# Kernel tuning notes

Hardware: AMD Instinct MI355X
Metric: run time of the kernel (lower is better)

The kernel has to match this reference:

```python
import jax, jax.numpy as jnp
import numpy as np
from jax import lax

N, D, NUM_SPEC, NUM_HOPS = 8192, 256, 32, 3
ETA, EPS, LN_EPS = 0.5, 0.5, 1e-5


def setup_inputs() -> dict:
    key = jax.random.key(0)
    ks = jax.random.split(key, 4)
    H = jax.random.normal(ks[0], (N, D), dtype=jnp.float32)
    # normalized adjacency proxy: scale so spectral norm is O(1) and hops stay stable
    A = jax.random.normal(ks[1], (N, N), dtype=jnp.float32) / jnp.sqrt(jnp.float32(N))
    # orthonormal-ish eigenvector columns
    V = jax.random.normal(ks[2], (N, NUM_SPEC), dtype=jnp.float32)
    V = V / jnp.linalg.norm(V, axis=0, keepdims=True)
    eigvals = jax.random.uniform(ks[3], (NUM_SPEC,), dtype=jnp.float32, maxval=2.0)
    return {
        "H": H,
        "A": A,
        "V": V,
        "eigvals": eigvals,
        "spec_logits": jnp.zeros((NUM_SPEC,), jnp.float32),
        "lap_logits": jnp.full((NUM_SPEC,), 0.1, jnp.float32),
        "hop_weights": jnp.full((NUM_HOPS + 1,), 1.0 / (NUM_HOPS + 1), jnp.float32),
        "threshold": jnp.full((D,), 0.05, jnp.float32),
        "ln_gamma": jnp.ones((D,), jnp.float32),
        "ln_beta": jnp.zeros((D,), jnp.float32),
    }


def reference(H, A, V, eigvals, spec_logits, lap_logits, hop_weights, threshold, ln_gamma, ln_beta):
    n, d = H.shape
    num_hops = hop_weights.shape[0] - 1

    # hop propagation: hops[k] = A^k H, shape [K, n, d] with K = num_hops+1
    def step(Hc, _):
        Hn = A @ Hc
        return Hn, Hn
    _, rest = lax.scan(step, H, None, length=num_hops)
    hops = jnp.concatenate([H[None], rest], axis=0)  # [K, n, d]

    hop_w = jax.nn.softmax(hop_weights)          # [K]
    spec_w = jax.nn.softmax(spec_logits)         # [S]
    lap_lams = jax.nn.softplus(lap_logits)       # [S]
    coeff = jnp.float32(d) / (jnp.float32(n) * jnp.float32(EPS) ** 2)

    # Phi[k,s,:] = v_s^T H_k  -> batched rank-1 projections
    Phi = jnp.einsum('ns,knd->ksd', V, hops)     # [K, S, d]

    # M = I + coeff * phi phi^T, batched small [d,d] SPD solves
    eye = jnp.eye(d, dtype=H.dtype)
    M = eye + coeff * jnp.einsum('ksi,ksj->ksij', Phi, Phi)  # [K,S,d,d]
    # phi @ M^{-1} == M^{-1} phi (M symmetric)
    q = coeff * jnp.linalg.solve(M, Phi[..., None])[..., 0]  # [K,S,d]

    # grad_R_total = sum_{k,s} hop_w[k] spec_w[s] v_s q_{k,s}^T = V @ T_R
    T_R = spec_w[:, None] * jnp.einsum('k,ksd->sd', hop_w, q)       # [S,d]
    grad_R = V @ T_R                                                 # [n,d]

    # grad_L_total = sum_{k,s} hop_w[k] lap_lams[s] eig_s v_s phi_{k,s}^T
    T_L = (lap_lams * eigvals)[:, None] * jnp.einsum('k,ksd->sd', hop_w, Phi)
    grad_L = V @ T_L

    H_half = H + ETA * grad_R - ETA * grad_L

    # soft threshold (proximal L1)
    thr = threshold[None, :]
    H_out = jnp.sign(H_half) * jax.nn.relu(jnp.abs(H_half) - thr)

    # LayerNorm over last dim
    mu = jnp.mean(H_out, axis=-1, keepdims=True)
    var = jnp.var(H_out, axis=-1, keepdims=True)
    H_out = (H_out - mu) / jnp.sqrt(var + LN_EPS) * ln_gamma + ln_beta
    return (H_out, lax.stop_gradient(hop_w), lax.stop_gradient(spec_w))
```

## Files before the change

### kernel.cpp

```cpp
#include <hip/hip_runtime.h>
#include <hip/hip_bf16.h>
#include <stdint.h>

#define NN 8192
#define DIM 256
#define NSPEC 32
#define ETA 0.5f
#define COEFF 0.125f
#define LNEPS 1e-5f

typedef __attribute__((ext_vector_type(8))) short bf16x8;
typedef __attribute__((ext_vector_type(4))) float f32x4;

__device__ __forceinline__ unsigned short bf2u(__hip_bfloat16 b) {
    union { __hip_bfloat16 b; unsigned short u; } c; c.b = b; return c.u;
}
__device__ __forceinline__ __hip_bfloat16 u2bf(unsigned short u) {
    union { __hip_bfloat16 b; unsigned short u; } c; c.u = u; return c.b;
}
__device__ __forceinline__ float bfbits2f(unsigned short u) {
    union { unsigned int i; float f; } c; c.i = ((unsigned int)u) << 16; return c.f;
}

__device__ __forceinline__ void async16(const void* g, void* l) {
    __builtin_amdgcn_global_load_lds(
        (const __attribute__((address_space(1))) void*)g,
        (__attribute__((address_space(3))) void*)l, 16, 0, 0);
}

__global__ void cast_A(const float4* __restrict__ src, ushort4* __restrict__ dst, int n4) {
    int i = blockIdx.x * 256 + threadIdx.x;
    int stride = gridDim.x * 256;
    for (int j = i; j < n4; j += stride) {
        float4 v = src[j];
        ushort4 o;
        o.x = bf2u(__float2bfloat16(v.x));
        o.y = bf2u(__float2bfloat16(v.y));
        o.z = bf2u(__float2bfloat16(v.z));
        o.w = bf2u(__float2bfloat16(v.w));
        dst[j] = o;
    }
}

__global__ void cast_trans(const float* __restrict__ X, __hip_bfloat16* __restrict__ Xbf,
                           __hip_bfloat16* __restrict__ XT) {
    __shared__ unsigned short tile[64 * 66];
    int r0 = blockIdx.x * 64, c0 = blockIdx.y * 64;
    int t = threadIdx.x;
    for (int i = 0; i < 16; ++i) {
        int idx = i * 256 + t;
        int r = idx >> 6, c = idx & 63;
        float v = X[(long)(r0 + r) * DIM + c0 + c];
        __hip_bfloat16 b = __float2bfloat16(v);
        Xbf[(long)(r0 + r) * DIM + c0 + c] = b;
        tile[r * 66 + c] = bf2u(b);
    }
    __syncthreads();
    for (int i = 0; i < 16; ++i) {
        int idx = i * 256 + t;
        int c = idx >> 6, r = idx & 63;
        XT[(long)(c0 + c) * NN + r0 + r] = u2bf(tile[r * 66 + c]);
    }
}

#define BM 128
#define BN 128
#define BK 64
#define KSPLIT 4
#define KC (NN / KSPLIT)
#define KITERS (KC / BK)

__launch_bounds__(256, 2)
__global__ void gemm_splitk(const __hip_bfloat16* __restrict__ A,
                            const __hip_bfloat16* __restrict__ BT,
                            float* __restrict__ P) {
    __shared__ __align__(16) __hip_bfloat16 As[2][BM * BK];
    __shared__ __align__(16) __hip_bfloat16 Bs[2][BN * BK];
    const int t = threadIdx.x;
    const int w = t >> 6, l = t & 63;
    const int wm = w & 1, wn = w >> 1;
    const long gm0 = (long)blockIdx.x * BM;
    const long gn0 = (long)blockIdx.y * BN;
    const long kbase = (long)blockIdx.z * KC;

    const int lr = l >> 3;
    const int lg = l & 7;
    const int glog = lg ^ lr;

    auto stage = [&](int buf, long kpos) {
#pragma unroll
        for (int c = 0; c < 4; ++c) {
            int rb = w * 32 + c * 8;
            async16(A + (gm0 + rb + lr) * (long)NN + kpos + glog * 8, &As[buf][rb * BK]);
        }
#pragma unroll
        for (int c = 0; c < 4; ++c) {
            int rb = w * 32 + c * 8;
            async16(BT + (gn0 + rb + lr) * (long)NN + kpos + glog * 8, &Bs[buf][rb * BK]);
        }
    };

    f32x4 acc[4][4];
#pragma unroll
    for (int mt = 0; mt < 4; ++mt)
#pragma unroll
        for (int nt = 0; nt < 4; ++nt)
            acc[mt][nt] = (f32x4){0.f, 0.f, 0.f, 0.f};

    const int rowq = l & 15;
    const int kq = l >> 4;

    stage(0, kbase);
    for (int kt = 0; kt < KITERS; ++kt) {
        __syncthreads();
        const int cur = kt & 1;
        if (kt + 1 < KITERS) stage(cur ^ 1, kbase + (long)(kt + 1) * BK);

#pragma unroll
        for (int ks = 0; ks < 2; ++ks) {
            const int kg = kq + ks * 4;
            bf16x8 af[4], bfr[4];
#pragma unroll
            for (int mt = 0; mt < 4; ++mt) {
                int m = wm * 64 + mt * 16 + rowq;
                af[mt] = *(const bf16x8*)&As[cur][m * BK + ((kg ^ (m & 7)) << 3)];
            }
#pragma unroll
            for (int nt = 0; nt < 4; ++nt) {
                int n = wn * 64 + nt * 16 + rowq;
                bfr[nt] = *(const bf16x8*)&Bs[cur][n * BK + ((kg ^ (n & 7)) << 3)];
            }
#pragma unroll
            for (int mt = 0; mt < 4; ++mt)
#pragma unroll
                for (int nt = 0; nt < 4; ++nt)
                    acc[mt][nt] = __builtin_amdgcn_mfma_f32_16x16x32_bf16(
                        af[mt], bfr[nt], acc[mt][nt], 0, 0, 0);
        }
    }

    float* Pz = P + (long)blockIdx.z * NN * DIM;
#pragma unroll
    for (int mt = 0; mt < 4; ++mt)
#pragma unroll
        for (int nt = 0; nt < 4; ++nt)
#pragma unroll
            for (int r = 0; r < 4; ++r) {
                long m = gm0 + wm * 64 + mt * 16 + (l >> 4) * 4 + r;
                long n = gn0 + wn * 64 + nt * 16 + (l & 15);
                Pz[m * DIM + n] = acc[mt][nt][r];
            }
}

__global__ void reduce_ct(const float* __restrict__ P, __hip_bfloat16* __restrict__ Xbf,
                          __hip_bfloat16* __restrict__ XT, int writeT) {
    __shared__ unsigned short tile[64 * 66];
    int r0 = blockIdx.x * 64, c0 = blockIdx.y * 64;
    int t = threadIdx.x;
    const long S = (long)NN * DIM;
    for (int i = 0; i < 16; ++i) {
        int idx = i * 256 + t;
        int r = idx >> 6, c = idx & 63;
        long off = (long)(r0 + r) * DIM + c0 + c;
        float v = P[off] + P[S + off] + P[2 * S + off] + P[3 * S + off];
        __hip_bfloat16 b = __float2bfloat16(v);
        Xbf[off] = b;
        tile[r * 66 + c] = bf2u(b);
    }
    __syncthreads();
    if (writeT) {
        for (int i = 0; i < 16; ++i) {
            int idx = i * 256 + t;
            int c = idx >> 6, r = idx & 63;
            XT[(long)(c0 + c) * NN + r0 + r] = u2bf(tile[r * 66 + c]);
        }
    }
}

__global__ void phi_kernel(const float* __restrict__ V,
                           const __hip_bfloat16* __restrict__ X0,
                           const __hip_bfloat16* __restrict__ X1,
                           const __hip_bfloat16* __restrict__ X2,
                           const __hip_bfloat16* __restrict__ X3,
                           float* __restrict__ Phi) {
    __shared__ float ldsV[64 * NSPEC];
    int t = threadIdx.x;
    int s0 = (t >> 6) * 8;
    int d0 = (t & 63) * 4;
    int n0 = blockIdx.x * 128;
    int k = blockIdx.y;
    const __hip_bfloat16* X = (k == 0) ? X0 : (k == 1) ? X1 : (k == 2) ? X2 : X3;
    float4 acc[8];
#pragma unroll
    for (int j = 0; j < 8; ++j) acc[j] = (float4){0.f, 0.f, 0.f, 0.f};

    for (int tile = 0; tile < 2; ++tile) {
        int nb = n0 + tile * 64;
#pragma unroll
        for (int i = 0; i < 8; ++i) {
            int idx = i * 256 + t;
            int r = idx >> 5, c = idx & 31;
            ldsV[idx] = V[(long)(nb + r) * NSPEC + c];
        }
        __syncthreads();
        for (int nn = 0; nn < 64; ++nn) {
            ushort4 xu = *(const ushort4*)&X[(long)(nb + nn) * DIM + d0];
            float x0 = bfbits2f(xu.x), x1 = bfbits2f(xu.y), x2 = bfbits2f(xu.z), x3 = bfbits2f(xu.w);
#pragma unroll
            for (int j = 0; j < 8; ++j) {
                float vs = ldsV[nn * NSPEC + s0 + j];
                acc[j].x += vs * x0; acc[j].y += vs * x1;
                acc[j].z += vs * x2; acc[j].w += vs * x3;
            }
        }
        __syncthreads();
    }
#pragma unroll
    for (int j = 0; j < 8; ++j) {
        float* ph = &Phi[((k * NSPEC) + s0 + j) * DIM + d0];
        atomicAdd(ph + 0, acc[j].x);
        atomicAdd(ph + 1, acc[j].y);
        atomicAdd(ph + 2, acc[j].z);
        atomicAdd(ph + 3, acc[j].w);
    }
}

__global__ void tc_kernel(const float* __restrict__ Phi,
                          const float* __restrict__ eigvals,
                          const float* __restrict__ spec_logits,
                          const float* __restrict__ lap_logits,
                          const float* __restrict__ hop_weights,
                          float* __restrict__ Tc,
                          float* __restrict__ out_tail) {
    int s = blockIdx.x, t = threadIdx.x;
    float hw0 = hop_weights[0], hw1 = hop_weights[1], hw2 = hop_weights[2], hw3 = hop_weights[3];
    float hm = fmaxf(fmaxf(hw0, hw1), fmaxf(hw2, hw3));
    hw0 = expf(hw0 - hm); hw1 = expf(hw1 - hm); hw2 = expf(hw2 - hm); hw3 = expf(hw3 - hm);
    float hs = hw0 + hw1 + hw2 + hw3;
    hw0 /= hs; hw1 /= hs; hw2 /= hs; hw3 /= hs;
    float hw[4] = {hw0, hw1, hw2, hw3};
    float sm = -1e30f;
    for (int j = 0; j < NSPEC; ++j) sm = fmaxf(sm, spec_logits[j]);
    float ssum = 0.f;
    for (int j = 0; j < NSPEC; ++j) ssum += expf(spec_logits[j] - sm);
    float spec_w_s = expf(spec_logits[s] - sm) / ssum;
    float lp = lap_logits[s];
    float lap = (lp > 20.f) ? lp : log1pf(expf(lp));
    float le = lap * eigvals[s];

    __shared__ float red[4];
    float accR = 0.f, accL = 0.f;
    for (int k = 0; k < 4; ++k) {
        float phi = Phi[(k * NSPEC + s) * DIM + t];
        float v = phi * phi;
        for (int off = 32; off; off >>= 1) v += __shfl_xor(v, off);
        if ((t & 63) == 0) red[t >> 6] = v;
        __syncthreads();
        float ssq = red[0] + red[1] + red[2] + red[3];
        __syncthreads();
        float q = COEFF * phi / (1.f + COEFF * ssq);
        accR += hw[k] * q;
        accL += hw[k] * phi;
    }
    Tc[s * DIM + t] = spec_w_s * accR - le * accL;
    if (s == 0) {
        if (t < 4) out_tail[t] = hw[t];
        if (t < NSPEC) out_tail[4 + t] = expf(spec_logits[t] - sm) / ssum;
    }
}

__launch_bounds__(256)
__global__ void final_kernel(const float* __restrict__ H, const float* __restrict__ V,
                             const float* __restrict__ Tc, const float* __restrict__ thr,
                             const float* __restrict__ gamma, const float* __restrict__ beta,
                             float* __restrict__ out) {
    __shared__ float tc[NSPEC * DIM];
    int t = threadIdx.x;
    {
        const float4* s4 = (const float4*)Tc;
        float4* d4 = (float4*)tc;
        for (int i = 0; i < 8; ++i) d4[i * 256 + t] = s4[i * 256 + t];
    }
    __syncthreads();
    int w = t >> 6, l = t & 63;
    long row = (long)blockIdx.x * 4 + w;
    int d0 = l * 4;
    const float* vrow = V + row * NSPEC;
    float4 G = {0.f, 0.f, 0.f, 0.f};
#pragma unroll 8
    for (int s = 0; s < NSPEC; ++s) {
        float vs = vrow[s];
        float4 c4 = *(const float4*)&tc[s * DIM + d0];
        G.x += vs * c4.x; G.y += vs * c4.y; G.z += vs * c4.z; G.w += vs * c4.w;
    }
    float4 h = *(const float4*)&H[row * DIM + d0];
    float4 th = *(const float4*)&thr[d0];
    float y[4];
    y[0] = h.x + ETA * G.x; y[1] = h.y + ETA * G.y;
    y[2] = h.z + ETA * G.z; y[3] = h.w + ETA * G.w;
    float tv[4] = {th.x, th.y, th.z, th.w};
    float s1 = 0.f, s2 = 0.f;
#pragma unroll
    for (int j = 0; j < 4; ++j) {
        float a = fabsf(y[j]) - tv[j];
        y[j] = (a > 0.f) ? copysignf(a, y[j]) : 0.f;
        s1 += y[j];
        s2 += y[j] * y[j];
    }
    for (int off = 32; off; off >>= 1) { s1 += __shfl_xor(s1, off); s2 += __shfl_xor(s2, off); }
    float mean = s1 * (1.f / DIM);
    float var = s2 * (1.f / DIM) - mean * mean;
    float inv = rsqrtf(var + LNEPS);
    float4 g4 = *(const float4*)&gamma[d0];
    float4 b4 = *(const float4*)&beta[d0];
    float4 o;
    o.x = (y[0] - mean) * inv * g4.x + b4.x;
    o.y = (y[1] - mean) * inv * g4.y + b4.y;
    o.z = (y[2] - mean) * inv * g4.z + b4.z;
    o.w = (y[3] - mean) * inv * g4.w + b4.w;
    *(float4*)&out[row * DIM + d0] = o;
}

extern "C" void kernel_launch(void* const* d_in, const int* in_sizes, int n_in,
                              void* d_out, int out_size, void* d_ws, size_t ws_size,
                              hipStream_t stream) {
    const float* H = (const float*)d_in[0];
    const float* A = (const float*)d_in[1];
    const float* V = (const float*)d_in[2];
    const float* eigvals = (const float*)d_in[3];
    const float* spec_logits = (const float*)d_in[4];
    const float* lap_logits = (const float*)d_in[5];
    const float* hop_weights = (const float*)d_in[6];
    const float* threshold = (const float*)d_in[7];
    const float* ln_gamma = (const float*)d_in[8];
    const float* ln_beta = (const float*)d_in[9];

    char* ws = (char*)d_ws;
    __hip_bfloat16* Abf  = (__hip_bfloat16*)ws;
    __hip_bfloat16* H0bf = (__hip_bfloat16*)(ws + 134217728);
    __hip_bfloat16* H0T  = (__hip_bfloat16*)(ws + 138412032);
    float*          P    = (float*)(ws + 142606336);
    __hip_bfloat16* C1   = (__hip_bfloat16*)(ws + 176160768);
    __hip_bfloat16* C1T  = (__hip_bfloat16*)(ws + 180355072);
    __hip_bfloat16* C2   = (__hip_bfloat16*)(ws + 184549376);
    __hip_bfloat16* C2T  = (__hip_bfloat16*)(ws + 188743680);
    __hip_bfloat16* C3   = (__hip_bfloat16*)(ws + 192937984);
    float* Phi = (float*)(ws + 197132288);
    float* Tc  = (float*)(ws + 197263360);
    float* out = (float*)d_out;

    hipMemsetAsync(Phi, 0, 4 * NSPEC * DIM * sizeof(float), stream);
    cast_A<<<4096, 256, 0, stream>>>((const float4*)A, (ushort4*)Abf, NN * NN / 4);
    cast_trans<<<dim3(128, 4), 256, 0, stream>>>(H, H0bf, H0T);

    gemm_splitk<<<dim3(64, 2, KSPLIT), 256, 0, stream>>>(Abf, H0T, P);
    reduce_ct<<<dim3(128, 4), 256, 0, stream>>>(P, C1, C1T, 1);
    gemm_splitk<<<dim3(64, 2, KSPLIT), 256, 0, stream>>>(Abf, C1T, P);
    reduce_ct<<<dim3(128, 4), 256, 0, stream>>>(P, C2, C2T, 1);
    gemm_splitk<<<dim3(64, 2, KSPLIT), 256, 0, stream>>>(Abf, C2T, P);
    reduce_ct<<<dim3(128, 4), 256, 0, stream>>>(P, C3, C3, 0);

    phi_kernel<<<dim3(64, 4), 256, 0, stream>>>(V, H0bf, C1, C2, C3, Phi);
    tc_kernel<<<NSPEC, 256, 0, stream>>>(Phi, eigvals, spec_logits, lap_logits, hop_weights,
                                         Tc, out + (long)NN * DIM);
    final_kernel<<<2048, 256, 0, stream>>>(H, V, Tc, threshold, ln_gamma, ln_beta, out);
}
```

Measured before the change: 681.5 us.

## Propagate eigenvectors through A^T instead of features through A

```diff
diff --git a/kernel.cpp b/kernel.cpp
--- a/kernel.cpp
+++ b/kernel.cpp
@@ -18,9 +18,6 @@
 __device__ __forceinline__ __hip_bfloat16 u2bf(unsigned short u) {
     union { __hip_bfloat16 b; unsigned short u; } c; c.u = u; return c.b;
 }
-__device__ __forceinline__ float bfbits2f(unsigned short u) {
-    union { unsigned int i; float f; } c; c.i = ((unsigned int)u) << 16; return c.f;
-}
 
 __device__ __forceinline__ void async16(const void* g, void* l) {
     __builtin_amdgcn_global_load_lds(
@@ -28,168 +25,146 @@
         (__attribute__((address_space(3))) void*)l, 16, 0, 0);
 }
 
-__global__ void cast_A(const float4* __restrict__ src, ushort4* __restrict__ dst, int n4) {
-    int i = blockIdx.x * 256 + threadIdx.x;
-    int stride = gridDim.x * 256;
-    for (int j = i; j < n4; j += stride) {
-        float4 v = src[j];
-        ushort4 o;
-        o.x = bf2u(__float2bfloat16(v.x));
-        o.y = bf2u(__float2bfloat16(v.y));
-        o.z = bf2u(__float2bfloat16(v.z));
-        o.w = bf2u(__float2bfloat16(v.w));
-        dst[j] = o;
-    }
-}
-
-__global__ void cast_trans(const float* __restrict__ X, __hip_bfloat16* __restrict__ Xbf,
-                           __hip_bfloat16* __restrict__ XT) {
+__global__ void castT_A(const float* __restrict__ A, __hip_bfloat16* __restrict__ AT) {
     __shared__ unsigned short tile[64 * 66];
     int r0 = blockIdx.x * 64, c0 = blockIdx.y * 64;
     int t = threadIdx.x;
     for (int i = 0; i < 16; ++i) {
         int idx = i * 256 + t;
         int r = idx >> 6, c = idx & 63;
-        float v = X[(long)(r0 + r) * DIM + c0 + c];
-        __hip_bfloat16 b = __float2bfloat16(v);
-        Xbf[(long)(r0 + r) * DIM + c0 + c] = b;
-        tile[r * 66 + c] = bf2u(b);
+        tile[r * 66 + c] = bf2u(__float2bfloat16(A[(long)(r0 + r) * NN + c0 + c]));
     }
     __syncthreads();
     for (int i = 0; i < 16; ++i) {
         int idx = i * 256 + t;
         int c = idx >> 6, r = idx & 63;
-        XT[(long)(c0 + c) * NN + r0 + r] = u2bf(tile[r * 66 + c]);
+        AT[(long)(c0 + c) * NN + r0 + r] = u2bf(tile[r * 66 + c]);
+    }
+}
+
+__global__ void trans_V(const float* __restrict__ V, __hip_bfloat16* __restrict__ VT) {
+    __shared__ float tile[64 * 33];
+    int n0 = blockIdx.x * 64;
+    int t = threadIdx.x;
+    for (int i = 0; i < 8; ++i) {
+        int idx = i * 256 + t;
+        tile[(idx >> 5) * 33 + (idx & 31)] = V[(long)(n0 + (idx >> 5)) * NSPEC + (idx & 31)];
+    }
+    __syncthreads();
+    for (int i = 0; i < 8; ++i) {
+        int idx = i * 256 + t;
+        int s = idx >> 6, r = idx & 63;
+        VT[(long)s * NN + n0 + r] = __float2bfloat16(tile[r * 33 + s]);
     }
 }
 
 #define BM 128
-#define BN 128
-#define BK 64
-#define KSPLIT 4
-#define KC (NN / KSPLIT)
-#define KITERS (KC / BK)
+#define BKH 128
+#define HSPLIT 8
+#define HKC (NN / HSPLIT)
+#define HITERS (HKC / BKH)
 
 __launch_bounds__(256, 2)
-__global__ void gemm_splitk(const __hip_bfloat16* __restrict__ A,
-                            const __hip_bfloat16* __restrict__ BT,
-                            float* __restrict__ P) {
-    __shared__ __align__(16) __hip_bfloat16 As[2][BM * BK];
-    __shared__ __align__(16) __hip_bfloat16 Bs[2][BN * BK];
+__global__ void gemm_hopW(const __hip_bfloat16* __restrict__ AT,
+                          const __hip_bfloat16* __restrict__ WT,
+                          float* __restrict__ P) {
+    __shared__ __align__(16) __hip_bfloat16 As[2][BM * BKH];
+    __shared__ __align__(16) __hip_bfloat16 Ws[2][NSPEC * BKH];
     const int t = threadIdx.x;
     const int w = t >> 6, l = t & 63;
     const int wm = w & 1, wn = w >> 1;
     const long gm0 = (long)blockIdx.x * BM;
-    const long gn0 = (long)blockIdx.y * BN;
-    const long kbase = (long)blockIdx.z * KC;
-
-    const int lr = l >> 3;
-    const int lg = l & 7;
-    const int glog = lg ^ lr;
+    const long kbase = (long)blockIdx.y * HKC;
+
+    const int lr4 = l >> 4;
+    const int lg = l & 15;
 
     auto stage = [&](int buf, long kpos) {
 #pragma unroll
-        for (int c = 0; c < 4; ++c) {
-            int rb = w * 32 + c * 8;
-            async16(A + (gm0 + rb + lr) * (long)NN + kpos + glog * 8, &As[buf][rb * BK]);
-        }
-#pragma unroll
-        for (int c = 0; c < 4; ++c) {
-            int rb = w * 32 + c * 8;
-            async16(BT + (gn0 + rb + lr) * (long)NN + kpos + glog * 8, &Bs[buf][rb * BK]);
+        for (int c = 0; c < 8; ++c) {
+            int rb = w * 32 + c * 4;
+            int row = rb + lr4;
+            async16(AT + (gm0 + row) * (long)NN + kpos + ((lg ^ (row & 15)) << 3),
+                    &As[buf][rb * BKH]);
+        }
+#pragma unroll
+        for (int c = 0; c < 2; ++c) {
+            int rb = w * 8 + c * 4;
+            int row = rb + lr4;
+            async16(WT + (long)row * NN + kpos + ((lg ^ (row & 15)) << 3),
+                    &Ws[buf][rb * BKH]);
         }
     };
 
-    f32x4 acc[4][4];
-#pragma unroll
-    for (int mt = 0; mt < 4; ++mt)
-#pragma unroll
-        for (int nt = 0; nt < 4; ++nt)
-            acc[mt][nt] = (f32x4){0.f, 0.f, 0.f, 0.f};
+    f32x4 acc[4];
+#pragma unroll
+    for (int mt = 0; mt < 4; ++mt) acc[mt] = (f32x4){0.f, 0.f, 0.f, 0.f};
 
     const int rowq = l & 15;
     const int kq = l >> 4;
 
     stage(0, kbase);
-    for (int kt = 0; kt < KITERS; ++kt) {
+    for (int kt = 0; kt < HITERS; ++kt) {
         __syncthreads();
         const int cur = kt & 1;
-        if (kt + 1 < KITERS) stage(cur ^ 1, kbase + (long)(kt + 1) * BK);
-
-#pragma unroll
-        for (int ks = 0; ks < 2; ++ks) {
-            const int kg = kq + ks * 4;
-            bf16x8 af[4], bfr[4];
+        if (kt + 1 < HITERS) stage(cur ^ 1, kbase + (long)(kt + 1) * BKH);
+
+#pragma unroll
+        for (int ks = 0; ks < 4; ++ks) {
+            const int pg = ((ks * 4 + kq) ^ rowq) << 3;
+            bf16x8 bfrag = *(const bf16x8*)&Ws[cur][(wn * 16 + rowq) * BKH + pg];
 #pragma unroll
             for (int mt = 0; mt < 4; ++mt) {
-                int m = wm * 64 + mt * 16 + rowq;
-                af[mt] = *(const bf16x8*)&As[cur][m * BK + ((kg ^ (m & 7)) << 3)];
+                bf16x8 afrag = *(const bf16x8*)&As[cur][(wm * 64 + mt * 16 + rowq) * BKH + pg];
+                acc[mt] = __builtin_amdgcn_mfma_f32_16x16x32_bf16(afrag, bfrag, acc[mt], 0, 0, 0);
             }
-#pragma unroll
-            for (int nt = 0; nt < 4; ++nt) {
-                int n = wn * 64 + nt * 16 + rowq;
-                bfr[nt] = *(const bf16x8*)&Bs[cur][n * BK + ((kg ^ (n & 7)) << 3)];
-            }
-#pragma unroll
-            for (int mt = 0; mt < 4; ++mt)
-#pragma unroll
-                for (int nt = 0; nt < 4; ++nt)
-                    acc[mt][nt] = __builtin_amdgcn_mfma_f32_16x16x32_bf16(
-                        af[mt], bfr[nt], acc[mt][nt], 0, 0, 0);
-        }
-    }
-
-    float* Pz = P + (long)blockIdx.z * NN * DIM;
+        }
+    }
+
+    float* Pz = P + (long)blockIdx.y * NN * NSPEC;
+    const int s = wn * 16 + (l & 15);
 #pragma unroll
     for (int mt = 0; mt < 4; ++mt)
 #pragma unroll
-        for (int nt = 0; nt < 4; ++nt)
-#pragma unroll
-            for (int r = 0; r < 4; ++r) {
-                long m = gm0 + wm * 64 + mt * 16 + (l >> 4) * 4 + r;
-                long n = gn0 + wn * 64 + nt * 16 + (l & 15);
-                Pz[m * DIM + n] = acc[mt][nt][r];
-            }
-}
-
-__global__ void reduce_ct(const float* __restrict__ P, __hip_bfloat16* __restrict__ Xbf,
-                          __hip_bfloat16* __restrict__ XT, int writeT) {
-    __shared__ unsigned short tile[64 * 66];
-    int r0 = blockIdx.x * 64, c0 = blockIdx.y * 64;
-    int t = threadIdx.x;
-    const long S = (long)NN * DIM;
-    for (int i = 0; i < 16; ++i) {
-        int idx = i * 256 + t;
-        int r = idx >> 6, c = idx & 63;
-        long off = (long)(r0 + r) * DIM + c0 + c;
-        float v = P[off] + P[S + off] + P[2 * S + off] + P[3 * S + off];
-        __hip_bfloat16 b = __float2bfloat16(v);
-        Xbf[off] = b;
-        tile[r * 66 + c] = bf2u(b);
+        for (int r = 0; r < 4; ++r) {
+            long m = gm0 + wm * 64 + mt * 16 + (l >> 4) * 4 + r;
+            Pz[m * NSPEC + s] = acc[mt][r];
+        }
+}
+
+__global__ void reduce_W(const float* __restrict__ P, float* __restrict__ Wf,
+                         __hip_bfloat16* __restrict__ WTbf) {
+    __shared__ float tile[64 * 33];
+    int n0 = blockIdx.x * 64;
+    int t = threadIdx.x;
+    for (int i = 0; i < 8; ++i) {
+        int idx = i * 256 + t;
+        int r = idx >> 5, s = idx & 31;
+        long off = (long)(n0 + r) * NSPEC + s;
+        float v = 0.f;
+#pragma unroll
+        for (int z = 0; z < HSPLIT; ++z) v += P[(long)z * NN * NSPEC + off];
+        Wf[off] = v;
+        tile[r * 33 + s] = v;
     }
     __syncthreads();
-    if (writeT) {
-        for (int i = 0; i < 16; ++i) {
-            int idx = i * 256 + t;
-            int c = idx >> 6, r = idx & 63;
-            XT[(long)(c0 + c) * NN + r0 + r] = u2bf(tile[r * 66 + c]);
-        }
-    }
-}
-
-__global__ void phi_kernel(const float* __restrict__ V,
-                           const __hip_bfloat16* __restrict__ X0,
-                           const __hip_bfloat16* __restrict__ X1,
-                           const __hip_bfloat16* __restrict__ X2,
-                           const __hip_bfloat16* __restrict__ X3,
-                           float* __restrict__ Phi) {
-    __shared__ float ldsV[64 * NSPEC];
+    for (int i = 0; i < 8; ++i) {
+        int idx = i * 256 + t;
+        int s = idx >> 6, r = idx & 63;
+        WTbf[(long)s * NN + n0 + r] = __float2bfloat16(tile[r * 33 + s]);
+    }
+}
+
+__global__ void phi_kernel(const float* __restrict__ W0, const float* __restrict__ W1,
+                           const float* __restrict__ W2, const float* __restrict__ W3,
+                           const float* __restrict__ H, float* __restrict__ Phi) {
+    __shared__ float ldsW[64 * NSPEC];
     int t = threadIdx.x;
     int s0 = (t >> 6) * 8;
     int d0 = (t & 63) * 4;
     int n0 = blockIdx.x * 128;
     int k = blockIdx.y;
-    const __hip_bfloat16* X = (k == 0) ? X0 : (k == 1) ? X1 : (k == 2) ? X2 : X3;
+    const float* W = (k == 0) ? W0 : (k == 1) ? W1 : (k == 2) ? W2 : W3;
     float4 acc[8];
 #pragma unroll
     for (int j = 0; j < 8; ++j) acc[j] = (float4){0.f, 0.f, 0.f, 0.f};
@@ -199,18 +174,16 @@
 #pragma unroll
         for (int i = 0; i < 8; ++i) {
             int idx = i * 256 + t;
-            int r = idx >> 5, c = idx & 31;
-            ldsV[idx] = V[(long)(nb + r) * NSPEC + c];
+            ldsW[idx] = W[(long)(nb + (idx >> 5)) * NSPEC + (idx & 31)];
         }
         __syncthreads();
         for (int nn = 0; nn < 64; ++nn) {
-            ushort4 xu = *(const ushort4*)&X[(long)(nb + nn) * DIM + d0];
-            float x0 = bfbits2f(xu.x), x1 = bfbits2f(xu.y), x2 = bfbits2f(xu.z), x3 = bfbits2f(xu.w);
+            float4 x = *(const float4*)&H[(long)(nb + nn) * DIM + d0];
 #pragma unroll
             for (int j = 0; j < 8; ++j) {
-                float vs = ldsV[nn * NSPEC + s0 + j];
-                acc[j].x += vs * x0; acc[j].y += vs * x1;
-                acc[j].z += vs * x2; acc[j].w += vs * x3;
+                float vs = ldsW[nn * NSPEC + s0 + j];
+                acc[j].x += vs * x.x; acc[j].y += vs * x.y;
+                acc[j].z += vs * x.z; acc[j].w += vs * x.w;
             }
         }
         __syncthreads();
@@ -336,31 +309,31 @@
     const float* ln_beta = (const float*)d_in[9];
 
     char* ws = (char*)d_ws;
-    __hip_bfloat16* Abf  = (__hip_bfloat16*)ws;
-    __hip_bfloat16* H0bf = (__hip_bfloat16*)(ws + 134217728);
-    __hip_bfloat16* H0T  = (__hip_bfloat16*)(ws + 138412032);
-    float*          P    = (float*)(ws + 142606336);
-    __hip_bfloat16* C1   = (__hip_bfloat16*)(ws + 176160768);
-    __hip_bfloat16* C1T  = (__hip_bfloat16*)(ws + 180355072);
-    __hip_bfloat16* C2   = (__hip_bfloat16*)(ws + 184549376);
-    __hip_bfloat16* C2T  = (__hip_bfloat16*)(ws + 188743680);
-    __hip_bfloat16* C3   = (__hip_bfloat16*)(ws + 192937984);
-    float* Phi = (float*)(ws + 197132288);
-    float* Tc  = (float*)(ws + 197263360);
+    __hip_bfloat16* ATbf = (__hip_bfloat16*)ws;
+    float*          P    = (float*)(ws + 134217728);
+    __hip_bfloat16* VTbf = (__hip_bfloat16*)(ws + 142606336);
+    float* W1f = (float*)(ws + 143130624);
+    float* W2f = (float*)(ws + 144179200);
+    float* W3f = (float*)(ws + 145227776);
+    __hip_bfloat16* W1T = (__hip_bfloat16*)(ws + 146276352);
+    __hip_bfloat16* W2T = (__hip_bfloat16*)(ws + 146800640);
+    __hip_bfloat16* W3T = (__hip_bfloat16*)(ws + 147324928);
+    float* Phi = (float*)(ws + 147849216);
+    float* Tc  = (float*)(ws + 147980288);
     float* out = (float*)d_out;
 
     hipMemsetAsync(Phi, 0, 4 * NSPEC * DIM * sizeof(float), stream);
-    cast_A<<<4096, 256, 0, stream>>>((const float4*)A, (ushort4*)Abf, NN * NN / 4);
-    cast_trans<<<dim3(128, 4), 256, 0, stream>>>(H, H0bf, H0T);
-
-    gemm_splitk<<<dim3(64, 2, KSPLIT), 256, 0, stream>>>(Abf, H0T, P);
-    reduce_ct<<<dim3(128, 4), 256, 0, stream>>>(P, C1, C1T, 1);
-    gemm_splitk<<<dim3(64, 2, KSPLIT), 256, 0, stream>>>(Abf, C1T, P);
-    reduce_ct<<<dim3(128, 4), 256, 0, stream>>>(P, C2, C2T, 1);
-    gemm_splitk<<<dim3(64, 2, KSPLIT), 256, 0, stream>>>(Abf, C2T, P);
-    reduce_ct<<<dim3(128, 4), 256, 0, stream>>>(P, C3, C3, 0);
-
-    phi_kernel<<<dim3(64, 4), 256, 0, stream>>>(V, H0bf, C1, C2, C3, Phi);
+    castT_A<<<dim3(128, 128), 256, 0, stream>>>(A, ATbf);
+    trans_V<<<128, 256, 0, stream>>>(V, VTbf);
+
+    gemm_hopW<<<dim3(64, HSPLIT), 256, 0, stream>>>(ATbf, VTbf, P);
+    reduce_W<<<128, 256, 0, stream>>>(P, W1f, W1T);
+    gemm_hopW<<<dim3(64, HSPLIT), 256, 0, stream>>>(ATbf, W1T, P);
+    reduce_W<<<128, 256, 0, stream>>>(P, W2f, W2T);
+    gemm_hopW<<<dim3(64, HSPLIT), 256, 0, stream>>>(ATbf, W2T, P);
+    reduce_W<<<128, 256, 0, stream>>>(P, W3f, W3T);
+
+    phi_kernel<<<dim3(64, 4), 256, 0, stream>>>(V, W1f, W2f, W3f, H, Phi);
     tc_kernel<<<NSPEC, 256, 0, stream>>>(Phi, eigvals, spec_logits, lap_logits, hop_weights,
                                          Tc, out + (long)NN * DIM);
     final_kernel<<<2048, 256, 0, stream>>>(H, V, Tc, threshold, ln_gamma, ln_beta, out);
```

New measurement: 601.1 us. 1.13x faster.
